# Performance work log

Hardware: AMD Instinct MI355X
Metric: run time of the kernel (lower is better)

Reference implementation:

```python
import jax, jax.numpy as jnp
import numpy as np

D_MODEL = 1024
D_FF = 4096
N_EXPERTS = 8
D_EXPERT = D_FF // N_EXPERTS  # 512
TOP_K = 2
LB_WEIGHT = 0.01
B, S = 4, 2048


def setup_inputs() -> dict:
    key = jax.random.key(0)
    ks = jax.random.split(key, 8)
    x = jax.random.normal(ks[0], (B, S, D_MODEL), dtype=jnp.float32)
    # per-expert FFN params stacked on expert axis
    w1 = jax.random.normal(ks[1], (N_EXPERTS, D_MODEL, D_EXPERT), dtype=jnp.float32) * (1.0 / np.sqrt(D_MODEL))
    b1 = jnp.zeros((N_EXPERTS, D_EXPERT), dtype=jnp.float32)
    w2 = jax.random.normal(ks[2], (N_EXPERTS, D_EXPERT, D_MODEL), dtype=jnp.float32) * (1.0 / np.sqrt(D_EXPERT))
    b2 = jnp.zeros((N_EXPERTS, D_MODEL), dtype=jnp.float32)
    centroids = jax.random.normal(ks[3], (N_EXPERTS, D_MODEL), dtype=jnp.float32) * 0.02
    w_route = jax.random.normal(ks[4], (N_EXPERTS, D_MODEL), dtype=jnp.float32) * (1.0 / np.sqrt(D_MODEL))
    return {"x": x, "w1": w1, "b1": b1, "w2": w2, "b2": b2,
            "centroids": centroids, "w_route": w_route}


def _top_k_softmax(logits, k):
    # softmax restricted to the top-k logits per token; zeros elsewhere
    vals, _ = jax.lax.top_k(logits, k)          # (..., k)
    thresh = vals[..., -1:]                     # kth-largest value
    masked = jnp.where(logits >= thresh, logits, -jnp.inf)
    return jax.nn.softmax(masked, axis=-1)


def reference(x, w1, b1, w2, b2, centroids, w_route):
    eps = 1e-12
    x_norm = x / jnp.maximum(jnp.linalg.norm(x, axis=-1, keepdims=True), eps)
    c_norm = centroids / jnp.maximum(jnp.linalg.norm(centroids, axis=-1, keepdims=True), eps)
    cos_scores = jnp.einsum('bsd,ed->bse', x_norm, c_norm)
    route_scores = jnp.einsum('bsd,ed->bse', x, w_route)
    logits = cos_scores + route_scores                       # (B,S,E)
    gates = _top_k_softmax(logits, TOP_K)                    # (B,S,E)
    # all experts computed on all tokens (dense MoE, masked combine)
    h = jax.nn.gelu(jnp.einsum('bsd,edh->bseh', x, w1) + b1, approximate=False)
    expert_out = jnp.einsum('bseh,ehd->bsed', h, w2) + b2    # (B,S,E,D)
    out = jnp.einsum('bse,bsed->bsd', gates, expert_out)
    return out
```

## Files before the change

### kernel.cpp

```cpp
#include <hip/hip_runtime.h>
#include <hip/hip_bf16.h>
#include <math.h>

#define T_TOK 8192
#define DM 1024
#define DE 512
#define NE 8
#define DFF 4096

#define CO_X   0
#define CO_W1  8388608
#define CO_W2  12582912
#define CO_B1  16777216
#define CO_B2  16781312
#define CO_CE  16789504
#define CO_WR  16797696
#define CO_TOT 16805888

#define WS_GATE2 256
#define WS_B32   65792
#define WS_TOP2  262400
#define WS_TOK   295168
#define WS_AE    360704
#define WS_AG    426240
#define WS_INV   491776
#define WS_CONV  557312
#define WS_HC    34169088
#define WS_OC    50946304

typedef __attribute__((ext_vector_type(8))) __bf16 bf16x8;
typedef __attribute__((ext_vector_type(4))) __bf16 bf16x4;
typedef __attribute__((ext_vector_type(8))) unsigned short u16x8;
typedef __attribute__((ext_vector_type(4))) float f32x4;
typedef __attribute__((ext_vector_type(4))) unsigned int u32x4;

__device__ __forceinline__ f32x4 ld4(const void* p, size_t off, int md)
{
  f32x4 r;
  if (md){
    bf16x4 v = *(const bf16x4*)((const __bf16*)p + off);
    #pragma unroll
    for (int j = 0; j < 4; j++) r[j] = (float)v[j];
  } else {
    r = *(const f32x4*)((const float*)p + off);
  }
  return r;
}

__global__ __launch_bounds__(256) void detect_k(const void* xp, const void* cp,
                                                int* meta, int* b32)
{
  const int tid = threadIdx.x;
  const float* xf = (const float*)xp;
  int ok = 0;
  for (int i = tid; i < 1024; i += 256){
    float a = fabsf(xf[i]);
    if (a > 1e-8f && a < 100.f) ok++;
  }
  __shared__ int cnt;
  __shared__ int flg;
  if (tid == 0) cnt = 0;
  __syncthreads();
  atomicAdd(&cnt, ok);
  __syncthreads();
  if (tid == 0){ flg = (cnt > 512) ? 0 : 1; meta[0] = flg; }
  __syncthreads();
  const int md = flg;

  const int e = tid >> 5, i = tid & 31;
  float ss = 0.f;
  for (int j = 0; j < 32; j++){
    size_t d = (size_t)e * DM + i + j * 32;
    float v = md ? (float)((const __bf16*)cp)[d] : ((const float*)cp)[d];
    ss += v * v;
  }
  #pragma unroll
  for (int m = 1; m < 32; m <<= 1) ss += __shfl_xor(ss, m, 64);
  float* cinv = (float*)(meta + 48);
  if (i == 0) cinv[e] = 1.f / fmaxf(sqrtf(ss), 1e-12f);

  b32[tid] = 0;
  if (tid < 8) meta[16 + tid] = 0;
}

__global__ __launch_bounds__(256) void convert_k(
    const float* __restrict__ x, const float* __restrict__ w1,
    const float* __restrict__ b1, const float* __restrict__ w2,
    const float* __restrict__ b2, const float* __restrict__ ce,
    const float* __restrict__ wr, __bf16* __restrict__ dst,
    const int* __restrict__ meta)
{
  if (meta[0]) return;
  const size_t i = ((size_t)blockIdx.x * 256 + threadIdx.x) * 4;
  const float* src; size_t off;
  if      (i < CO_W1){ src = x;  off = i - CO_X;  }
  else if (i < CO_W2){ src = w1; off = i - CO_W1; }
  else if (i < CO_B1){ src = w2; off = i - CO_W2; }
  else if (i < CO_B2){ src = b1; off = i - CO_B1; }
  else if (i < CO_CE){ src = b2; off = i - CO_B2; }
  else if (i < CO_WR){ src = ce; off = i - CO_CE; }
  else               { src = wr; off = i - CO_WR; }
  f32x4 v = *(const f32x4*)(src + off);
  bf16x4 o;
  #pragma unroll
  for (int j = 0; j < 4; j++) o[j] = (__bf16)v[j];
  *(bf16x4*)(dst + i) = o;
}

__global__ __launch_bounds__(256) void route_k(
    const void* __restrict__ xp, const void* __restrict__ cp,
    const void* __restrict__ wp, const int* __restrict__ meta,
    float2* __restrict__ gate2, int* __restrict__ top2, int* __restrict__ b32)
{
  const int md = meta[0];
  const float* cinv = (const float*)(meta + 48);
  const int tid = threadIdx.x;
  const int g = tid >> 4, l = tid & 15;
  const int t = blockIdx.x * 16 + g;

  __shared__ int hist[8];
  if (tid < 8) hist[tid] = 0;
  __syncthreads();

  float xx = 0.f, cd[NE], wd[NE];
  #pragma unroll
  for (int e = 0; e < NE; e++){ cd[e] = 0.f; wd[e] = 0.f; }

  const size_t xbase = (size_t)t * DM;
  for (int j = 0; j < 16; j++){
    const int d0 = j * 64 + l * 4;
    f32x4 xv = ld4(xp, xbase + d0, md);
    xx += xv[0]*xv[0] + xv[1]*xv[1] + xv[2]*xv[2] + xv[3]*xv[3];
    #pragma unroll
    for (int e = 0; e < NE; e++){
      f32x4 cv = ld4(cp, (size_t)e * DM + d0, md);
      f32x4 wv = ld4(wp, (size_t)e * DM + d0, md);
      cd[e] += xv[0]*cv[0] + xv[1]*cv[1] + xv[2]*cv[2] + xv[3]*cv[3];
      wd[e] += xv[0]*wv[0] + xv[1]*wv[1] + xv[2]*wv[2] + xv[3]*wv[3];
    }
  }
  #pragma unroll
  for (int m = 1; m < 16; m <<= 1){
    xx += __shfl_xor(xx, m, 64);
    #pragma unroll
    for (int e = 0; e < NE; e++){
      cd[e] += __shfl_xor(cd[e], m, 64);
      wd[e] += __shfl_xor(wd[e], m, 64);
    }
  }

  if (l == 0){
    const float rxn = 1.f / fmaxf(sqrtf(xx), 1e-12f);
    float logits[NE];
    #pragma unroll
    for (int e = 0; e < NE; e++) logits[e] = cd[e] * rxn * cinv[e] + wd[e];
    float m1 = -1e30f; int i1 = 0;
    #pragma unroll
    for (int e = 0; e < NE; e++) if (logits[e] > m1){ m1 = logits[e]; i1 = e; }
    float m2 = -1e30f; int i2 = (i1 == 0) ? 1 : 0;
    #pragma unroll
    for (int e = 0; e < NE; e++)
      if (e != i1 && logits[e] > m2){ m2 = logits[e]; i2 = e; }
    float denom = 0.f, ex1 = 0.f, ex2 = 0.f;
    #pragma unroll
    for (int e = 0; e < NE; e++){
      if (logits[e] >= m2){
        float ee = expf(logits[e] - m1);
        denom += ee;
        if (e == i1) ex1 = ee;
        if (e == i2) ex2 = ee;
      }
    }
    const float inv = 1.f / denom;
    gate2[t] = make_float2(ex1 * inv, ex2 * inv);
    top2[t] = i1 | (i2 << 8);
    atomicAdd(&hist[i1], 1);
    atomicAdd(&hist[i2], 1);
  }
  __syncthreads();
  if (tid < 8) atomicAdd(&b32[(blockIdx.x >> 4) * 8 + tid], hist[tid]);
}

__global__ void offsets_k(int* meta, int* b32)
{
  const int l = threadIdx.x;
  int running = 0;
  for (int e = 0; e < NE; e++){
    int v = (l < 32) ? b32[l * 8 + e] : 0;
    int incl = v;
    #pragma unroll
    for (int ofs = 1; ofs < 32; ofs <<= 1){
      int n = __shfl_up(incl, ofs, 64);
      if (l >= ofs) incl += n;
    }
    int tot = __shfl(incl, 31, 64);
    if (l < 32) b32[l * 8 + e] = running + (incl - v);
    if (l == 0){ meta[16 + e] = tot; meta[32 + e] = running; }
    running += tot;
  }
}

__global__ __launch_bounds__(256) void place_k(
    const int* __restrict__ top2, const float2* __restrict__ gate2,
    const int* __restrict__ b32, int* __restrict__ tok, int* __restrict__ ae,
    float* __restrict__ agv, int* __restrict__ inv)
{
  __shared__ int cur[8];
  if (threadIdx.x < 8) cur[threadIdx.x] = b32[blockIdx.x * 8 + threadIdx.x];
  __syncthreads();
  const int t = blockIdx.x * 256 + threadIdx.x;
  const int p = top2[t];
  const float2 gg = gate2[t];
  const int e1 = p & 255, e2 = (p >> 8) & 255;
  const int s1 = atomicAdd(&cur[e1], 1);
  tok[s1] = t; ae[s1] = e1; agv[s1] = gg.x; inv[2 * t] = s1;
  const int s2 = atomicAdd(&cur[e2], 1);
  tok[s2] = t; ae[s2] = e2; agv[s2] = gg.y; inv[2 * t + 1] = s2;
}

__device__ __forceinline__ bool find_tile(const int* meta, int tm,
                                          int& e, int& base, int& valid)
{
  for (e = 0; e < NE; e++){
    const int cnt = meta[16 + e];
    const int nt = (cnt + 127) >> 7;
    if (tm < nt){
      const int r0 = tm << 7;
      base = meta[32 + e] + r0;
      valid = cnt - r0;
      return true;
    }
    tm -= nt;
  }
  return false;
}

__global__ __launch_bounds__(256) void gemm1g_k(
    const void* xq, const void* w1q, const void* b1q,
    const __bf16* __restrict__ conv, const int* __restrict__ meta,
    const int* __restrict__ tok, const float* __restrict__ agv,
    __bf16* __restrict__ Hc)
{
  const int md = meta[0];
  const __bf16* X  = md ? (const __bf16*)xq  : conv + CO_X;
  const __bf16* W  = md ? (const __bf16*)w1q : conv + CO_W1;
  const __bf16* bb = md ? (const __bf16*)b1q : conv + CO_B1;

  int e, base, valid;
  if (!find_tile(meta, blockIdx.x, e, base, valid)) return;
  const int n0 = blockIdx.y * 128;

  __shared__ __attribute__((aligned(16))) __bf16 As[128 * 40];
  __shared__ __attribute__((aligned(16))) unsigned int Bs[128 * 20];

  const int tid = threadIdx.x;
  const int wv = tid >> 6, lane = tid & 63;
  const int q = lane >> 4, ln = lane & 15;
  const int wm = (wv >> 1) * 64, wn = (wv & 1) * 64;
  f32x4 acc[4][4] = {};

  const int arow = tid >> 1, aseg = (tid & 1) * 16;
  const int gr = (arow < valid) ? arow : 0;
  const int trow = tok[base + gr];
  const __bf16* Ag = X + (size_t)trow * DM + aseg;

  const int bkp = tid & 15, bnc = (tid >> 4) * 8;
  const __bf16* Bg = W + (size_t)e * (DM * DE) + n0 + (size_t)(2 * bkp) * DE + bnc;

  for (int k0 = 0; k0 < DM; k0 += 32){
    *(bf16x8*)&As[arow * 40 + aseg]     = *(const bf16x8*)(Ag + k0);
    *(bf16x8*)&As[arow * 40 + aseg + 8] = *(const bf16x8*)(Ag + k0 + 8);
    bf16x8 r0v = *(const bf16x8*)(Bg + (size_t)k0 * DE);
    bf16x8 r1v = *(const bf16x8*)(Bg + (size_t)k0 * DE + DE);
    u16x8 s0 = __builtin_bit_cast(u16x8, r0v);
    u16x8 s1 = __builtin_bit_cast(u16x8, r1v);
    #pragma unroll
    for (int j = 0; j < 8; j++)
      Bs[(bnc + j) * 20 + bkp] = (unsigned)s0[j] | ((unsigned)s1[j] << 16);
    __syncthreads();

    bf16x8 af[4], bfv[4];
    #pragma unroll
    for (int mi = 0; mi < 4; mi++)
      af[mi] = *(const bf16x8*)&As[(wm + mi * 16 + ln) * 40 + q * 8];
    #pragma unroll
    for (int ni = 0; ni < 4; ni++){
      u32x4 bw = *(const u32x4*)&Bs[(wn + ni * 16 + ln) * 20 + q * 4];
      bfv[ni] = __builtin_bit_cast(bf16x8, bw);
    }
    #pragma unroll
    for (int mi = 0; mi < 4; mi++)
      #pragma unroll
      for (int ni = 0; ni < 4; ni++)
        acc[mi][ni] = __builtin_amdgcn_mfma_f32_16x16x32_bf16(
            af[mi], bfv[ni], acc[mi][ni], 0, 0, 0);
    __syncthreads();
  }

  const int coln = n0 + wn;
  float bset[4];
  #pragma unroll
  for (int ni = 0; ni < 4; ni++)
    bset[ni] = (float)bb[e * DE + coln + ni * 16 + ln];
  #pragma unroll
  for (int mi = 0; mi < 4; mi++){
    #pragma unroll
    for (int r = 0; r < 4; r++){
      const int row = wm + mi * 16 + q * 4 + r;
      if (row < valid){
        const int slot = base + row;
        const float g = agv[slot];
        #pragma unroll
        for (int ni = 0; ni < 4; ni++){
          float v = acc[mi][ni][r] + bset[ni];
          float h = 0.5f * v * (1.0f + erff(v * 0.70710678118654752f));
          Hc[(size_t)slot * DE + coln + ni * 16 + ln] = (__bf16)(g * h);
        }
      }
    }
  }
}

__global__ __launch_bounds__(256) void gemm2g_k(
    const __bf16* __restrict__ Hc, const void* w2q,
    const __bf16* __restrict__ conv, const int* __restrict__ meta,
    __bf16* __restrict__ Oc)
{
  const int md = meta[0];
  const __bf16* W = md ? (const __bf16*)w2q : conv + CO_W2;

  int e, base, valid;
  if (!find_tile(meta, blockIdx.x, e, base, valid)) return;
  const int n0 = blockIdx.y * 128;

  __shared__ __attribute__((aligned(16))) __bf16 As[128 * 40];
  __shared__ __attribute__((aligned(16))) unsigned int Bs[128 * 20];

  const int tid = threadIdx.x;
  const int wv = tid >> 6, lane = tid & 63;
  const int q = lane >> 4, ln = lane & 15;
  const int wm = (wv >> 1) * 64, wn = (wv & 1) * 64;
  f32x4 acc[4][4] = {};

  const int arow = tid >> 1, aseg = (tid & 1) * 16;
  const int gr = (arow < valid) ? arow : 0;
  const __bf16* Ag = Hc + (size_t)(base + gr) * DE + aseg;

  const int bkp = tid & 15, bnc = (tid >> 4) * 8;
  const __bf16* Bg = W + (size_t)e * (DE * DM) + n0 + (size_t)(2 * bkp) * DM + bnc;

  for (int k0 = 0; k0 < DE; k0 += 32){
    *(bf16x8*)&As[arow * 40 + aseg]     = *(const bf16x8*)(Ag + k0);
    *(bf16x8*)&As[arow * 40 + aseg + 8] = *(const bf16x8*)(Ag + k0 + 8);
    bf16x8 r0v = *(const bf16x8*)(Bg + (size_t)k0 * DM);
    bf16x8 r1v = *(const bf16x8*)(Bg + (size_t)k0 * DM + DM);
    u16x8 s0 = __builtin_bit_cast(u16x8, r0v);
    u16x8 s1 = __builtin_bit_cast(u16x8, r1v);
    #pragma unroll
    for (int j = 0; j < 8; j++)
      Bs[(bnc + j) * 20 + bkp] = (unsigned)s0[j] | ((unsigned)s1[j] << 16);
    __syncthreads();

    bf16x8 af[4], bfv[4];
    #pragma unroll
    for (int mi = 0; mi < 4; mi++)
      af[mi] = *(const bf16x8*)&As[(wm + mi * 16 + ln) * 40 + q * 8];
    #pragma unroll
    for (int ni = 0; ni < 4; ni++){
      u32x4 bw = *(const u32x4*)&Bs[(wn + ni * 16 + ln) * 20 + q * 4];
      bfv[ni] = __builtin_bit_cast(bf16x8, bw);
    }
    #pragma unroll
    for (int mi = 0; mi < 4; mi++)
      #pragma unroll
      for (int ni = 0; ni < 4; ni++)
        acc[mi][ni] = __builtin_amdgcn_mfma_f32_16x16x32_bf16(
            af[mi], bfv[ni], acc[mi][ni], 0, 0, 0);
    __syncthreads();
  }

  #pragma unroll
  for (int mi = 0; mi < 4; mi++){
    #pragma unroll
    for (int r = 0; r < 4; r++){
      const int row = wm + mi * 16 + q * 4 + r;
      if (row < valid){
        const int slot = base + row;
        #pragma unroll
        for (int ni = 0; ni < 4; ni++)
          Oc[(size_t)slot * DM + n0 + wn + ni * 16 + ln] = (__bf16)acc[mi][ni][r];
      }
    }
  }
}

__global__ __launch_bounds__(256) void combine_k(
    const __bf16* __restrict__ Oc, const int* __restrict__ inv,
    const int* __restrict__ ae, const float* __restrict__ agv,
    const void* b2q, const int* __restrict__ meta, void* out)
{
  const int md = meta[0];
  const int t = blockIdx.x;
  const int s1 = inv[2 * t], s2 = inv[2 * t + 1];
  const int e1 = ae[s1], e2 = ae[s2];
  const float g1 = agv[s1], g2 = agv[s2];
  const int c = threadIdx.x * 4;

  bf16x4 o1 = *(const bf16x4*)(Oc + (size_t)s1 * DM + c);
  bf16x4 o2 = *(const bf16x4*)(Oc + (size_t)s2 * DM + c);
  float b1v[4], b2v[4];
  if (md){
    const __bf16* B2 = (const __bf16*)b2q;
    bf16x4 a = *(const bf16x4*)(B2 + e1 * DM + c);
    bf16x4 b = *(const bf16x4*)(B2 + e2 * DM + c);
    #pragma unroll
    for (int j = 0; j < 4; j++){ b1v[j] = (float)a[j]; b2v[j] = (float)b[j]; }
  } else {
    const float* B2 = (const float*)b2q;
    f32x4 a = *(const f32x4*)(B2 + e1 * DM + c);
    f32x4 b = *(const f32x4*)(B2 + e2 * DM + c);
    #pragma unroll
    for (int j = 0; j < 4; j++){ b1v[j] = a[j]; b2v[j] = b[j]; }
  }
  f32x4 rr;
  #pragma unroll
  for (int j = 0; j < 4; j++)
    rr[j] = (float)o1[j] + (float)o2[j] + g1 * b1v[j] + g2 * b2v[j];

  if (md){
    bf16x4 ob;
    #pragma unroll
    for (int j = 0; j < 4; j++) ob[j] = (__bf16)rr[j];
    *(bf16x4*)((__bf16*)out + (size_t)t * DM + c) = ob;
  } else {
    *(f32x4*)((float*)out + (size_t)t * DM + c) = rr;
  }
}

extern "C" void kernel_launch(void* const* d_in, const int* in_sizes, int n_in,
                              void* d_out, int out_size, void* d_ws, size_t ws_size,
                              hipStream_t stream)
{
  char* ws = (char*)d_ws;
  int*    meta  = (int*)ws;
  float2* gate2 = (float2*)(ws + WS_GATE2);
  int*    b32   = (int*)(ws + WS_B32);
  int*    top2  = (int*)(ws + WS_TOP2);
  int*    tok   = (int*)(ws + WS_TOK);
  int*    ae    = (int*)(ws + WS_AE);
  float*  agv   = (float*)(ws + WS_AG);
  int*    inv   = (int*)(ws + WS_INV);
  __bf16* conv  = (__bf16*)(ws + WS_CONV);
  __bf16* Hc    = (__bf16*)(ws + WS_HC);
  __bf16* Oc    = (__bf16*)(ws + WS_OC);

  detect_k<<<1, 256, 0, stream>>>(d_in[0], d_in[5], meta, b32);
  convert_k<<<CO_TOT / 1024, 256, 0, stream>>>(
      (const float*)d_in[0], (const float*)d_in[1], (const float*)d_in[2],
      (const float*)d_in[3], (const float*)d_in[4], (const float*)d_in[5],
      (const float*)d_in[6], conv, meta);
  route_k<<<T_TOK / 16, 256, 0, stream>>>(d_in[0], d_in[5], d_in[6], meta,
                                          gate2, top2, b32);
  offsets_k<<<1, 64, 0, stream>>>(meta, b32);
  place_k<<<T_TOK / 256, 256, 0, stream>>>(top2, gate2, b32, tok, ae, agv, inv);
  gemm1g_k<<<dim3(136, 4), 256, 0, stream>>>(d_in[0], d_in[1], d_in[2], conv,
                                             meta, tok, agv, Hc);
  gemm2g_k<<<dim3(136, 8), 256, 0, stream>>>(Hc, d_in[3], conv, meta, Oc);
  combine_k<<<T_TOK, 256, 0, stream>>>(Oc, inv, ae, agv, d_in[4], meta, d_out);
}
```

Before: 260.7 us.

## Fuse combine into gemm2 via float atomics and halve GEMM N tiles

Drops the bf16 Oc intermediate and the combine kernel. A new init kernel writes the gated b2 bias into the output, and gemm2 then atomically adds its fp32 results into the output rows of each token. Both grouped GEMMs also move from 128x128 to 128x64 tiles, which doubles the grid to fill more CUs. The cost is fp32 atomics on global memory, a full output write in the init kernel, and less reuse per tile. The atomic path always writes fp32 output, so it ignores the bf16 output mode the old combine handled.

```diff
diff --git a/kernel.cpp b/kernel.cpp
--- a/kernel.cpp
+++ b/kernel.cpp
@@ -26,11 +26,10 @@
 #define WS_INV   491776
 #define WS_CONV  557312
 #define WS_HC    34169088
-#define WS_OC    50946304
 
 typedef __attribute__((ext_vector_type(8))) __bf16 bf16x8;
 typedef __attribute__((ext_vector_type(4))) __bf16 bf16x4;
-typedef __attribute__((ext_vector_type(8))) unsigned short u16x8;
+typedef __attribute__((ext_vector_type(4))) unsigned short u16x4;
 typedef __attribute__((ext_vector_type(4))) float f32x4;
 typedef __attribute__((ext_vector_type(4))) unsigned int u32x4;
 
@@ -218,6 +217,25 @@
   tok[s2] = t; ae[s2] = e2; agv[s2] = gg.y; inv[2 * t + 1] = s2;
 }
 
+__global__ __launch_bounds__(256) void out_init_k(
+    const int* __restrict__ top2, const float2* __restrict__ gate2,
+    const void* __restrict__ b2q, const int* __restrict__ meta,
+    float* __restrict__ out)
+{
+  const int md = meta[0];
+  const size_t idx = ((size_t)blockIdx.x * 256 + threadIdx.x) * 4;
+  const int t = (int)(idx >> 10), d = (int)(idx & 1023);
+  const int p = top2[t];
+  const float2 g = gate2[t];
+  const int e1 = p & 255, e2 = (p >> 8) & 255;
+  f32x4 bv1 = ld4(b2q, (size_t)e1 * DM + d, md);
+  f32x4 bv2 = ld4(b2q, (size_t)e2 * DM + d, md);
+  f32x4 r;
+  #pragma unroll
+  for (int j = 0; j < 4; j++) r[j] = g.x * bv1[j] + g.y * bv2[j];
+  *(f32x4*)(out + idx) = r;
+}
+
 __device__ __forceinline__ bool find_tile(const int* meta, int tm,
                                           int& e, int& base, int& valid)
 {
@@ -248,59 +266,59 @@
 
   int e, base, valid;
   if (!find_tile(meta, blockIdx.x, e, base, valid)) return;
-  const int n0 = blockIdx.y * 128;
+  const int n0 = blockIdx.y * 64;
 
   __shared__ __attribute__((aligned(16))) __bf16 As[128 * 40];
-  __shared__ __attribute__((aligned(16))) unsigned int Bs[128 * 20];
+  __shared__ __attribute__((aligned(16))) unsigned int Bs[64 * 20];
 
   const int tid = threadIdx.x;
   const int wv = tid >> 6, lane = tid & 63;
   const int q = lane >> 4, ln = lane & 15;
-  const int wm = (wv >> 1) * 64, wn = (wv & 1) * 64;
-  f32x4 acc[4][4] = {};
+  const int wm = (wv & 1) * 64, wn = (wv >> 1) * 32;
+  f32x4 acc[4][2] = {};
 
   const int arow = tid >> 1, aseg = (tid & 1) * 16;
   const int gr = (arow < valid) ? arow : 0;
   const int trow = tok[base + gr];
   const __bf16* Ag = X + (size_t)trow * DM + aseg;
 
-  const int bkp = tid & 15, bnc = (tid >> 4) * 8;
+  const int bkp = tid & 15, bnc = (tid >> 4) * 4;
   const __bf16* Bg = W + (size_t)e * (DM * DE) + n0 + (size_t)(2 * bkp) * DE + bnc;
 
   for (int k0 = 0; k0 < DM; k0 += 32){
     *(bf16x8*)&As[arow * 40 + aseg]     = *(const bf16x8*)(Ag + k0);
     *(bf16x8*)&As[arow * 40 + aseg + 8] = *(const bf16x8*)(Ag + k0 + 8);
-    bf16x8 r0v = *(const bf16x8*)(Bg + (size_t)k0 * DE);
-    bf16x8 r1v = *(const bf16x8*)(Bg + (size_t)k0 * DE + DE);
-    u16x8 s0 = __builtin_bit_cast(u16x8, r0v);
-    u16x8 s1 = __builtin_bit_cast(u16x8, r1v);
-    #pragma unroll
-    for (int j = 0; j < 8; j++)
+    bf16x4 r0v = *(const bf16x4*)(Bg + (size_t)k0 * DE);
+    bf16x4 r1v = *(const bf16x4*)(Bg + (size_t)k0 * DE + DE);
+    u16x4 s0 = __builtin_bit_cast(u16x4, r0v);
+    u16x4 s1 = __builtin_bit_cast(u16x4, r1v);
+    #pragma unroll
+    for (int j = 0; j < 4; j++)
       Bs[(bnc + j) * 20 + bkp] = (unsigned)s0[j] | ((unsigned)s1[j] << 16);
     __syncthreads();
 
-    bf16x8 af[4], bfv[4];
+    bf16x8 af[4], bfv[2];
     #pragma unroll
     for (int mi = 0; mi < 4; mi++)
       af[mi] = *(const bf16x8*)&As[(wm + mi * 16 + ln) * 40 + q * 8];
     #pragma unroll
-    for (int ni = 0; ni < 4; ni++){
+    for (int ni = 0; ni < 2; ni++){
       u32x4 bw = *(const u32x4*)&Bs[(wn + ni * 16 + ln) * 20 + q * 4];
       bfv[ni] = __builtin_bit_cast(bf16x8, bw);
     }
     #pragma unroll
     for (int mi = 0; mi < 4; mi++)
       #pragma unroll
-      for (int ni = 0; ni < 4; ni++)
+      for (int ni = 0; ni < 2; ni++)
         acc[mi][ni] = __builtin_amdgcn_mfma_f32_16x16x32_bf16(
             af[mi], bfv[ni], acc[mi][ni], 0, 0, 0);
     __syncthreads();
   }
 
   const int coln = n0 + wn;
-  float bset[4];
-  #pragma unroll
-  for (int ni = 0; ni < 4; ni++)
+  float bset[2];
+  #pragma unroll
+  for (int ni = 0; ni < 2; ni++)
     bset[ni] = (float)bb[e * DE + coln + ni * 16 + ln];
   #pragma unroll
   for (int mi = 0; mi < 4; mi++){
@@ -311,7 +329,7 @@
         const int slot = base + row;
         const float g = agv[slot];
         #pragma unroll
-        for (int ni = 0; ni < 4; ni++){
+        for (int ni = 0; ni < 2; ni++){
           float v = acc[mi][ni][r] + bset[ni];
           float h = 0.5f * v * (1.0f + erff(v * 0.70710678118654752f));
           Hc[(size_t)slot * DE + coln + ni * 16 + ln] = (__bf16)(g * h);
@@ -324,56 +342,56 @@
 __global__ __launch_bounds__(256) void gemm2g_k(
     const __bf16* __restrict__ Hc, const void* w2q,
     const __bf16* __restrict__ conv, const int* __restrict__ meta,
-    __bf16* __restrict__ Oc)
+    const int* __restrict__ tok, float* __restrict__ out)
 {
   const int md = meta[0];
   const __bf16* W = md ? (const __bf16*)w2q : conv + CO_W2;
 
   int e, base, valid;
   if (!find_tile(meta, blockIdx.x, e, base, valid)) return;
-  const int n0 = blockIdx.y * 128;
+  const int n0 = blockIdx.y * 64;
 
   __shared__ __attribute__((aligned(16))) __bf16 As[128 * 40];
-  __shared__ __attribute__((aligned(16))) unsigned int Bs[128 * 20];
+  __shared__ __attribute__((aligned(16))) unsigned int Bs[64 * 20];
 
   const int tid = threadIdx.x;
   const int wv = tid >> 6, lane = tid & 63;
   const int q = lane >> 4, ln = lane & 15;
-  const int wm = (wv >> 1) * 64, wn = (wv & 1) * 64;
-  f32x4 acc[4][4] = {};
+  const int wm = (wv & 1) * 64, wn = (wv >> 1) * 32;
+  f32x4 acc[4][2] = {};
 
   const int arow = tid >> 1, aseg = (tid & 1) * 16;
   const int gr = (arow < valid) ? arow : 0;
   const __bf16* Ag = Hc + (size_t)(base + gr) * DE + aseg;
 
-  const int bkp = tid & 15, bnc = (tid >> 4) * 8;
+  const int bkp = tid & 15, bnc = (tid >> 4) * 4;
   const __bf16* Bg = W + (size_t)e * (DE * DM) + n0 + (size_t)(2 * bkp) * DM + bnc;
 
   for (int k0 = 0; k0 < DE; k0 += 32){
     *(bf16x8*)&As[arow * 40 + aseg]     = *(const bf16x8*)(Ag + k0);
     *(bf16x8*)&As[arow * 40 + aseg + 8] = *(const bf16x8*)(Ag + k0 + 8);
-    bf16x8 r0v = *(const bf16x8*)(Bg + (size_t)k0 * DM);
-    bf16x8 r1v = *(const bf16x8*)(Bg + (size_t)k0 * DM + DM);
-    u16x8 s0 = __builtin_bit_cast(u16x8, r0v);
-    u16x8 s1 = __builtin_bit_cast(u16x8, r1v);
-    #pragma unroll
-    for (int j = 0; j < 8; j++)
+    bf16x4 r0v = *(const bf16x4*)(Bg + (size_t)k0 * DM);
+    bf16x4 r1v = *(const bf16x4*)(Bg + (size_t)k0 * DM + DM);
+    u16x4 s0 = __builtin_bit_cast(u16x4, r0v);
+    u16x4 s1 = __builtin_bit_cast(u16x4, r1v);
+    #pragma unroll
+    for (int j = 0; j < 4; j++)
       Bs[(bnc + j) * 20 + bkp] = (unsigned)s0[j] | ((unsigned)s1[j] << 16);
     __syncthreads();
 
-    bf16x8 af[4], bfv[4];
+    bf16x8 af[4], bfv[2];
     #pragma unroll
     for (int mi = 0; mi < 4; mi++)
       af[mi] = *(const bf16x8*)&As[(wm + mi * 16 + ln) * 40 + q * 8];
     #pragma unroll
-    for (int ni = 0; ni < 4; ni++){
+    for (int ni = 0; ni < 2; ni++){
       u32x4 bw = *(const u32x4*)&Bs[(wn + ni * 16 + ln) * 20 + q * 4];
       bfv[ni] = __builtin_bit_cast(bf16x8, bw);
     }
     #pragma unroll
     for (int mi = 0; mi < 4; mi++)
       #pragma unroll
-      for (int ni = 0; ni < 4; ni++)
+      for (int ni = 0; ni < 2; ni++)
         acc[mi][ni] = __builtin_amdgcn_mfma_f32_16x16x32_bf16(
             af[mi], bfv[ni], acc[mi][ni], 0, 0, 0);
     __syncthreads();
@@ -385,55 +403,13 @@
     for (int r = 0; r < 4; r++){
       const int row = wm + mi * 16 + q * 4 + r;
       if (row < valid){
-        const int slot = base + row;
+        const int t = tok[base + row];
         #pragma unroll
-        for (int ni = 0; ni < 4; ni++)
-          Oc[(size_t)slot * DM + n0 + wn + ni * 16 + ln] = (__bf16)acc[mi][ni][r];
+        for (int ni = 0; ni < 2; ni++)
+          atomicAdd(&out[(size_t)t * DM + n0 + wn + ni * 16 + ln],
+                    acc[mi][ni][r]);
       }
     }
-  }
-}
-
-__global__ __launch_bounds__(256) void combine_k(
-    const __bf16* __restrict__ Oc, const int* __restrict__ inv,
-    const int* __restrict__ ae, const float* __restrict__ agv,
-    const void* b2q, const int* __restrict__ meta, void* out)
-{
-  const int md = meta[0];
-  const int t = blockIdx.x;
-  const int s1 = inv[2 * t], s2 = inv[2 * t + 1];
-  const int e1 = ae[s1], e2 = ae[s2];
-  const float g1 = agv[s1], g2 = agv[s2];
-  const int c = threadIdx.x * 4;
-
-  bf16x4 o1 = *(const bf16x4*)(Oc + (size_t)s1 * DM + c);
-  bf16x4 o2 = *(const bf16x4*)(Oc + (size_t)s2 * DM + c);
-  float b1v[4], b2v[4];
-  if (md){
-    const __bf16* B2 = (const __bf16*)b2q;
-    bf16x4 a = *(const bf16x4*)(B2 + e1 * DM + c);
-    bf16x4 b = *(const bf16x4*)(B2 + e2 * DM + c);
-    #pragma unroll
-    for (int j = 0; j < 4; j++){ b1v[j] = (float)a[j]; b2v[j] = (float)b[j]; }
-  } else {
-    const float* B2 = (const float*)b2q;
-    f32x4 a = *(const f32x4*)(B2 + e1 * DM + c);
-    f32x4 b = *(const f32x4*)(B2 + e2 * DM + c);
-    #pragma unroll
-    for (int j = 0; j < 4; j++){ b1v[j] = a[j]; b2v[j] = b[j]; }
-  }
-  f32x4 rr;
-  #pragma unroll
-  for (int j = 0; j < 4; j++)
-    rr[j] = (float)o1[j] + (float)o2[j] + g1 * b1v[j] + g2 * b2v[j];
-
-  if (md){
-    bf16x4 ob;
-    #pragma unroll
-    for (int j = 0; j < 4; j++) ob[j] = (__bf16)rr[j];
-    *(bf16x4*)((__bf16*)out + (size_t)t * DM + c) = ob;
-  } else {
-    *(f32x4*)((float*)out + (size_t)t * DM + c) = rr;
   }
 }
 
@@ -452,7 +428,6 @@
   int*    inv   = (int*)(ws + WS_INV);
   __bf16* conv  = (__bf16*)(ws + WS_CONV);
   __bf16* Hc    = (__bf16*)(ws + WS_HC);
-  __bf16* Oc    = (__bf16*)(ws + WS_OC);
 
   detect_k<<<1, 256, 0, stream>>>(d_in[0], d_in[5], meta, b32);
   convert_k<<<CO_TOT / 1024, 256, 0, stream>>>(
@@ -463,8 +438,10 @@
                                           gate2, top2, b32);
   offsets_k<<<1, 64, 0, stream>>>(meta, b32);
   place_k<<<T_TOK / 256, 256, 0, stream>>>(top2, gate2, b32, tok, ae, agv, inv);
-  gemm1g_k<<<dim3(136, 4), 256, 0, stream>>>(d_in[0], d_in[1], d_in[2], conv,
+  out_init_k<<<T_TOK * DM / 1024, 256, 0, stream>>>(top2, gate2, d_in[4], meta,
+                                                    (float*)d_out);
+  gemm1g_k<<<dim3(136, 8), 256, 0, stream>>>(d_in[0], d_in[1], d_in[2], conv,
                                              meta, tok, agv, Hc);
-  gemm2g_k<<<dim3(136, 8), 256, 0, stream>>>(Hc, d_in[3], conv, meta, Oc);
-  combine_k<<<T_TOK, 256, 0, stream>>>(Oc, inv, ae, agv, d_in[4], meta, d_out);
-}
+  gemm2g_k<<<dim3(136, 16), 256, 0, stream>>>(Hc, d_in[3], conv, meta, tok,
+                                              (float*)d_out);
+}
```

Measured after the change: 335.4 us. 28.7% more time.

## Pre-transpose expert weights and stage GEMM tiles via async global-to-LDS loads

Applied to the files above, without the earlier changes.

A new transpose kernel converts w1 and w2 to bf16 and stores them K-contiguous in the workspace, replacing the plain fp32-to-bf16 conversion of those weights. Both grouped GEMMs then copy A and B tiles straight into shared memory with global_load_lds, which removes the register round trip and the per-element B repacking. The unpadded 32-wide LDS layout may cause bank conflicts on fragment reads. There is still no double buffering, and the transpose adds a kernel on every call that also runs when inputs are already bf16.

```diff
diff --git a/kernel.cpp b/kernel.cpp
--- a/kernel.cpp
+++ b/kernel.cpp
@@ -30,9 +30,7 @@
 
 typedef __attribute__((ext_vector_type(8))) __bf16 bf16x8;
 typedef __attribute__((ext_vector_type(4))) __bf16 bf16x4;
-typedef __attribute__((ext_vector_type(8))) unsigned short u16x8;
 typedef __attribute__((ext_vector_type(4))) float f32x4;
-typedef __attribute__((ext_vector_type(4))) unsigned int u32x4;
 
 __device__ __forceinline__ f32x4 ld4(const void* p, size_t off, int md)
 {
@@ -45,6 +43,13 @@
     r = *(const f32x4*)((const float*)p + off);
   }
   return r;
+}
+
+__device__ __forceinline__ void async_ld16(const __bf16* g, __bf16* l)
+{
+  __builtin_amdgcn_global_load_lds(
+      (const __attribute__((address_space(1))) unsigned int*)g,
+      (__attribute__((address_space(3))) unsigned int*)l, 16, 0, 0);
 }
 
 __global__ __launch_bounds__(256) void detect_k(const void* xp, const void* cp,
@@ -84,27 +89,68 @@
 }
 
 __global__ __launch_bounds__(256) void convert_k(
-    const float* __restrict__ x, const float* __restrict__ w1,
-    const float* __restrict__ b1, const float* __restrict__ w2,
+    const float* __restrict__ x, const float* __restrict__ b1,
     const float* __restrict__ b2, const float* __restrict__ ce,
     const float* __restrict__ wr, __bf16* __restrict__ dst,
     const int* __restrict__ meta)
 {
   if (meta[0]) return;
   const size_t i = ((size_t)blockIdx.x * 256 + threadIdx.x) * 4;
-  const float* src; size_t off;
-  if      (i < CO_W1){ src = x;  off = i - CO_X;  }
-  else if (i < CO_W2){ src = w1; off = i - CO_W1; }
-  else if (i < CO_B1){ src = w2; off = i - CO_W2; }
-  else if (i < CO_B2){ src = b1; off = i - CO_B1; }
-  else if (i < CO_CE){ src = b2; off = i - CO_B2; }
-  else if (i < CO_WR){ src = ce; off = i - CO_CE; }
-  else               { src = wr; off = i - CO_WR; }
-  f32x4 v = *(const f32x4*)(src + off);
+  const float* src; size_t doff;
+  if (i < 8388608){ src = x + i; doff = CO_X + i; }
+  else {
+    size_t j = i - 8388608;
+    doff = CO_B1 + j;
+    if      (j < 4096)  src = b1 + j;
+    else if (j < 12288) src = b2 + (j - 4096);
+    else if (j < 20480) src = ce + (j - 12288);
+    else                src = wr + (j - 20480);
+  }
+  f32x4 v = *(const f32x4*)src;
   bf16x4 o;
   #pragma unroll
   for (int j = 0; j < 4; j++) o[j] = (__bf16)v[j];
-  *(bf16x4*)(dst + i) = o;
+  *(bf16x4*)(dst + doff) = o;
+}
+
+__global__ __launch_bounds__(256) void transp_k(
+    const void* w1q, const void* w2q, __bf16* __restrict__ conv,
+    const int* __restrict__ meta)
+{
+  const int md = meta[0];
+  __shared__ __bf16 tile[32][33];
+  const int b = blockIdx.x, tid = threadIdx.x;
+  const int ty = tid >> 5, tx = tid & 31;
+
+  const void* src; __bf16* dst; int ldS, ldD, i0, j0; size_t soff, doffb;
+  if (b < 4096){
+    const int e = b >> 9, t = b & 511;
+    i0 = (t >> 4) << 5; j0 = (t & 15) << 5;
+    ldS = DE; ldD = DM;
+    soff = (size_t)e * DM * DE;
+    dst = conv + CO_W1; doffb = (size_t)e * DE * DM;
+    src = md ? (const void*)((const __bf16*)w1q) : (const void*)((const float*)w1q);
+  } else {
+    const int e = (b - 4096) >> 9, t = (b - 4096) & 511;
+    i0 = (t >> 5) << 5; j0 = (t & 31) << 5;
+    ldS = DM; ldD = DE;
+    soff = (size_t)e * DE * DM;
+    dst = conv + CO_W2; doffb = (size_t)e * DM * DE;
+    src = md ? (const void*)((const __bf16*)w2q) : (const void*)((const float*)w2q);
+  }
+
+  #pragma unroll
+  for (int rr = 0; rr < 4; rr++){
+    const int r = rr * 8 + ty;
+    const size_t s = soff + (size_t)(i0 + r) * ldS + j0 + tx;
+    tile[r][tx] = md ? ((const __bf16*)src)[s] : (__bf16)((const float*)src)[s];
+  }
+  __syncthreads();
+  #pragma unroll
+  for (int rr = 0; rr < 4; rr++){
+    const int r = rr * 8 + ty;
+    dst[doffb + (size_t)(j0 + r) * ldD + i0 + tx] = tile[tx][r];
+  }
 }
 
 __global__ __launch_bounds__(256) void route_k(
@@ -236,22 +282,21 @@
 }
 
 __global__ __launch_bounds__(256) void gemm1g_k(
-    const void* xq, const void* w1q, const void* b1q,
-    const __bf16* __restrict__ conv, const int* __restrict__ meta,
-    const int* __restrict__ tok, const float* __restrict__ agv,
-    __bf16* __restrict__ Hc)
+    const void* xq, const void* b1q, const __bf16* __restrict__ conv,
+    const int* __restrict__ meta, const int* __restrict__ tok,
+    const float* __restrict__ agv, __bf16* __restrict__ Hc)
 {
   const int md = meta[0];
-  const __bf16* X  = md ? (const __bf16*)xq  : conv + CO_X;
-  const __bf16* W  = md ? (const __bf16*)w1q : conv + CO_W1;
+  const __bf16* X  = md ? (const __bf16*)xq : conv + CO_X;
+  const __bf16* WT = conv + CO_W1;
   const __bf16* bb = md ? (const __bf16*)b1q : conv + CO_B1;
 
   int e, base, valid;
   if (!find_tile(meta, blockIdx.x, e, base, valid)) return;
   const int n0 = blockIdx.y * 128;
 
-  __shared__ __attribute__((aligned(16))) __bf16 As[128 * 40];
-  __shared__ __attribute__((aligned(16))) unsigned int Bs[128 * 20];
+  __shared__ __attribute__((aligned(16))) __bf16 As[128 * 32];
+  __shared__ __attribute__((aligned(16))) __bf16 Bs[128 * 32];
 
   const int tid = threadIdx.x;
   const int wv = tid >> 6, lane = tid & 63;
@@ -259,42 +304,35 @@
   const int wm = (wv >> 1) * 64, wn = (wv & 1) * 64;
   f32x4 acc[4][4] = {};
 
-  const int arow = tid >> 1, aseg = (tid & 1) * 16;
-  const int gr = (arow < valid) ? arow : 0;
-  const int trow = tok[base + gr];
-  const __bf16* Ag = X + (size_t)trow * DM + aseg;
-
-  const int bkp = tid & 15, bnc = (tid >> 4) * 8;
-  const __bf16* Bg = W + (size_t)e * (DM * DE) + n0 + (size_t)(2 * bkp) * DE + bnc;
+  const int sr = tid >> 2, sc = (tid & 3) * 8;
+  const int t0 = tok[base + ((sr      < valid) ? sr      : 0)];
+  const int t1 = tok[base + ((sr + 64 < valid) ? sr + 64 : 0)];
+  const __bf16* Ag0 = X + (size_t)t0 * DM + sc;
+  const __bf16* Ag1 = X + (size_t)t1 * DM + sc;
+  const __bf16* Bg0 = WT + (size_t)e * (DE * DM) + (size_t)(n0 + sr) * DM + sc;
+  const __bf16* Bg1 = Bg0 + (size_t)64 * DM;
 
   for (int k0 = 0; k0 < DM; k0 += 32){
-    *(bf16x8*)&As[arow * 40 + aseg]     = *(const bf16x8*)(Ag + k0);
-    *(bf16x8*)&As[arow * 40 + aseg + 8] = *(const bf16x8*)(Ag + k0 + 8);
-    bf16x8 r0v = *(const bf16x8*)(Bg + (size_t)k0 * DE);
-    bf16x8 r1v = *(const bf16x8*)(Bg + (size_t)k0 * DE + DE);
-    u16x8 s0 = __builtin_bit_cast(u16x8, r0v);
-    u16x8 s1 = __builtin_bit_cast(u16x8, r1v);
-    #pragma unroll
-    for (int j = 0; j < 8; j++)
-      Bs[(bnc + j) * 20 + bkp] = (unsigned)s0[j] | ((unsigned)s1[j] << 16);
     __syncthreads();
-
-    bf16x8 af[4], bfv[4];
+    async_ld16(Ag0 + k0, As + tid * 8);
+    async_ld16(Ag1 + k0, As + 2048 + tid * 8);
+    async_ld16(Bg0 + k0, Bs + tid * 8);
+    async_ld16(Bg1 + k0, Bs + 2048 + tid * 8);
+    __syncthreads();
+
+    bf16x8 af[4], bf[4];
     #pragma unroll
     for (int mi = 0; mi < 4; mi++)
-      af[mi] = *(const bf16x8*)&As[(wm + mi * 16 + ln) * 40 + q * 8];
-    #pragma unroll
-    for (int ni = 0; ni < 4; ni++){
-      u32x4 bw = *(const u32x4*)&Bs[(wn + ni * 16 + ln) * 20 + q * 4];
-      bfv[ni] = __builtin_bit_cast(bf16x8, bw);
-    }
+      af[mi] = *(const bf16x8*)&As[(wm + mi * 16 + ln) * 32 + q * 8];
+    #pragma unroll
+    for (int ni = 0; ni < 4; ni++)
+      bf[ni] = *(const bf16x8*)&Bs[(wn + ni * 16 + ln) * 32 + q * 8];
     #pragma unroll
     for (int mi = 0; mi < 4; mi++)
       #pragma unroll
       for (int ni = 0; ni < 4; ni++)
         acc[mi][ni] = __builtin_amdgcn_mfma_f32_16x16x32_bf16(
-            af[mi], bfv[ni], acc[mi][ni], 0, 0, 0);
-    __syncthreads();
+            af[mi], bf[ni], acc[mi][ni], 0, 0, 0);
   }
 
   const int coln = n0 + wn;
@@ -322,19 +360,17 @@
 }
 
 __global__ __launch_bounds__(256) void gemm2g_k(
-    const __bf16* __restrict__ Hc, const void* w2q,
-    const __bf16* __restrict__ conv, const int* __restrict__ meta,
-    __bf16* __restrict__ Oc)
-{
-  const int md = meta[0];
-  const __bf16* W = md ? (const __bf16*)w2q : conv + CO_W2;
+    const __bf16* __restrict__ Hc, const __bf16* __restrict__ conv,
+    const int* __restrict__ meta, __bf16* __restrict__ Oc)
+{
+  const __bf16* WT = conv + CO_W2;
 
   int e, base, valid;
   if (!find_tile(meta, blockIdx.x, e, base, valid)) return;
   const int n0 = blockIdx.y * 128;
 
-  __shared__ __attribute__((aligned(16))) __bf16 As[128 * 40];
-  __shared__ __attribute__((aligned(16))) unsigned int Bs[128 * 20];
+  __shared__ __attribute__((aligned(16))) __bf16 As[128 * 32];
+  __shared__ __attribute__((aligned(16))) __bf16 Bs[128 * 32];
 
   const int tid = threadIdx.x;
   const int wv = tid >> 6, lane = tid & 63;
@@ -342,41 +378,35 @@
   const int wm = (wv >> 1) * 64, wn = (wv & 1) * 64;
   f32x4 acc[4][4] = {};
 
-  const int arow = tid >> 1, aseg = (tid & 1) * 16;
-  const int gr = (arow < valid) ? arow : 0;
-  const __bf16* Ag = Hc + (size_t)(base + gr) * DE + aseg;
-
-  const int bkp = tid & 15, bnc = (tid >> 4) * 8;
-  const __bf16* Bg = W + (size_t)e * (DE * DM) + n0 + (size_t)(2 * bkp) * DM + bnc;
+  const int sr = tid >> 2, sc = (tid & 3) * 8;
+  const int r0 = (sr      < valid) ? sr      : 0;
+  const int r1 = (sr + 64 < valid) ? sr + 64 : 0;
+  const __bf16* Ag0 = Hc + (size_t)(base + r0) * DE + sc;
+  const __bf16* Ag1 = Hc + (size_t)(base + r1) * DE + sc;
+  const __bf16* Bg0 = WT + (size_t)e * (DM * DE) + (size_t)(n0 + sr) * DE + sc;
+  const __bf16* Bg1 = Bg0 + (size_t)64 * DE;
 
   for (int k0 = 0; k0 < DE; k0 += 32){
-    *(bf16x8*)&As[arow * 40 + aseg]     = *(const bf16x8*)(Ag + k0);
-    *(bf16x8*)&As[arow * 40 + aseg + 8] = *(const bf16x8*)(Ag + k0 + 8);
-    bf16x8 r0v = *(const bf16x8*)(Bg + (size_t)k0 * DM);
-    bf16x8 r1v = *(const bf16x8*)(Bg + (size_t)k0 * DM + DM);
-    u16x8 s0 = __builtin_bit_cast(u16x8, r0v);
-    u16x8 s1 = __builtin_bit_cast(u16x8, r1v);
-    #pragma unroll
-    for (int j = 0; j < 8; j++)
-      Bs[(bnc + j) * 20 + bkp] = (unsigned)s0[j] | ((unsigned)s1[j] << 16);
     __syncthreads();
-
-    bf16x8 af[4], bfv[4];
+    async_ld16(Ag0 + k0, As + tid * 8);
+    async_ld16(Ag1 + k0, As + 2048 + tid * 8);
+    async_ld16(Bg0 + k0, Bs + tid * 8);
+    async_ld16(Bg1 + k0, Bs + 2048 + tid * 8);
+    __syncthreads();
+
+    bf16x8 af[4], bf[4];
     #pragma unroll
     for (int mi = 0; mi < 4; mi++)
-      af[mi] = *(const bf16x8*)&As[(wm + mi * 16 + ln) * 40 + q * 8];
-    #pragma unroll
-    for (int ni = 0; ni < 4; ni++){
-      u32x4 bw = *(const u32x4*)&Bs[(wn + ni * 16 + ln) * 20 + q * 4];
-      bfv[ni] = __builtin_bit_cast(bf16x8, bw);
-    }
+      af[mi] = *(const bf16x8*)&As[(wm + mi * 16 + ln) * 32 + q * 8];
+    #pragma unroll
+    for (int ni = 0; ni < 4; ni++)
+      bf[ni] = *(const bf16x8*)&Bs[(wn + ni * 16 + ln) * 32 + q * 8];
     #pragma unroll
     for (int mi = 0; mi < 4; mi++)
       #pragma unroll
       for (int ni = 0; ni < 4; ni++)
         acc[mi][ni] = __builtin_amdgcn_mfma_f32_16x16x32_bf16(
-            af[mi], bfv[ni], acc[mi][ni], 0, 0, 0);
-    __syncthreads();
+            af[mi], bf[ni], acc[mi][ni], 0, 0, 0);
   }
 
   #pragma unroll
@@ -408,24 +438,12 @@
 
   bf16x4 o1 = *(const bf16x4*)(Oc + (size_t)s1 * DM + c);
   bf16x4 o2 = *(const bf16x4*)(Oc + (size_t)s2 * DM + c);
-  float b1v[4], b2v[4];
-  if (md){
-    const __bf16* B2 = (const __bf16*)b2q;
-    bf16x4 a = *(const bf16x4*)(B2 + e1 * DM + c);
-    bf16x4 b = *(const bf16x4*)(B2 + e2 * DM + c);
-    #pragma unroll
-    for (int j = 0; j < 4; j++){ b1v[j] = (float)a[j]; b2v[j] = (float)b[j]; }
-  } else {
-    const float* B2 = (const float*)b2q;
-    f32x4 a = *(const f32x4*)(B2 + e1 * DM + c);
-    f32x4 b = *(const f32x4*)(B2 + e2 * DM + c);
-    #pragma unroll
-    for (int j = 0; j < 4; j++){ b1v[j] = a[j]; b2v[j] = b[j]; }
-  }
+  f32x4 bv1 = ld4(b2q, (size_t)e1 * DM + c, md);
+  f32x4 bv2 = ld4(b2q, (size_t)e2 * DM + c, md);
   f32x4 rr;
   #pragma unroll
   for (int j = 0; j < 4; j++)
-    rr[j] = (float)o1[j] + (float)o2[j] + g1 * b1v[j] + g2 * b2v[j];
+    rr[j] = (float)o1[j] + (float)o2[j] + g1 * bv1[j] + g2 * bv2[j];
 
   if (md){
     bf16x4 ob;
@@ -455,16 +473,16 @@
   __bf16* Oc    = (__bf16*)(ws + WS_OC);
 
   detect_k<<<1, 256, 0, stream>>>(d_in[0], d_in[5], meta, b32);
-  convert_k<<<CO_TOT / 1024, 256, 0, stream>>>(
-      (const float*)d_in[0], (const float*)d_in[1], (const float*)d_in[2],
-      (const float*)d_in[3], (const float*)d_in[4], (const float*)d_in[5],
-      (const float*)d_in[6], conv, meta);
+  transp_k<<<8192, 256, 0, stream>>>(d_in[1], d_in[3], conv, meta);
+  convert_k<<<8220, 256, 0, stream>>>(
+      (const float*)d_in[0], (const float*)d_in[2], (const float*)d_in[4],
+      (const float*)d_in[5], (const float*)d_in[6], conv, meta);
   route_k<<<T_TOK / 16, 256, 0, stream>>>(d_in[0], d_in[5], d_in[6], meta,
                                           gate2, top2, b32);
   offsets_k<<<1, 64, 0, stream>>>(meta, b32);
   place_k<<<T_TOK / 256, 256, 0, stream>>>(top2, gate2, b32, tok, ae, agv, inv);
-  gemm1g_k<<<dim3(136, 4), 256, 0, stream>>>(d_in[0], d_in[1], d_in[2], conv,
-                                             meta, tok, agv, Hc);
-  gemm2g_k<<<dim3(136, 8), 256, 0, stream>>>(Hc, d_in[3], conv, meta, Oc);
+  gemm1g_k<<<dim3(136, 4), 256, 0, stream>>>(d_in[0], d_in[2], conv, meta,
+                                             tok, agv, Hc);
+  gemm2g_k<<<dim3(136, 8), 256, 0, stream>>>(Hc, conv, meta, Oc);
   combine_k<<<T_TOK, 256, 0, stream>>>(Oc, inv, ae, agv, d_in[4], meta, d_out);
 }
```

After: 247.2 us. 5.2% less time.
